# Kernel tuning notes

Measured on AMD Instinct MI355X. Metric: run time of the kernel, lower is better.

The kernel has to match this reference:

```python
import jax, jax.numpy as jnp
import numpy as np

N_NODES = 100000
N_EDGES = 1600000
IN_F, HID, N_COLORS = 128, 128, 10


def setup_inputs() -> dict:
    key = jax.random.key(0)
    k1, k2, k3, k4 = jax.random.split(key, 4)
    x = jax.random.normal(k1, (N_NODES, IN_F), dtype=jnp.float32)
    edge_index = jax.random.randint(k2, (2, N_EDGES), 0, N_NODES, dtype=jnp.int64)
    # Glorot-ish init for weights
    W1 = jax.random.normal(k3, (IN_F, HID), dtype=jnp.float32) / np.sqrt(IN_F)
    b1 = jnp.zeros((HID,), dtype=jnp.float32)
    W2 = jax.random.normal(k4, (HID, N_COLORS), dtype=jnp.float32) / np.sqrt(HID)
    b2 = jnp.zeros((N_COLORS,), dtype=jnp.float32)
    return {"x": x, "edge_index": edge_index, "W1": W1, "b1": b1, "W2": W2, "b2": b2}


def _gcn_norm(edge_index, num_nodes):
    # Add self-loops, compute symmetric normalization D^-1/2 (A+I) D^-1/2
    loops = jnp.arange(num_nodes, dtype=edge_index.dtype)
    src = jnp.concatenate([edge_index[0], loops])
    dst = jnp.concatenate([edge_index[1], loops])
    deg = jax.ops.segment_sum(jnp.ones_like(dst, dtype=jnp.float32), dst,
                              num_segments=num_nodes)
    deg_isqrt = jax.lax.rsqrt(deg)  # deg >= 1 due to self-loops
    norm = deg_isqrt[src] * deg_isqrt[dst]  # [E + N]
    return src, dst, norm


def _gcn_conv(h, src, dst, norm, num_nodes, W, b):
    # Linear transform first (PyG GCNConv), then gather-scale-scatter aggregate
    h = h @ W                                   # [N, out]
    msg = h[src] * norm[:, None]                # [E + N, out] gather
    out = jax.ops.segment_sum(msg, dst, num_segments=num_nodes)  # scatter-add
    return out + b


def reference(x, edge_index, W1, b1, W2, b2):
    n = x.shape[0]
    src, dst, norm = _gcn_norm(edge_index, n)
    h = _gcn_conv(x, src, dst, norm, n, W1, b1)
    h = jax.nn.relu(h)
    # dropout is identity in eval mode
    h = _gcn_conv(h, src, dst, norm, n, W2, b2)
    return jax.nn.softmax(h, axis=1)
```

## Files before the change

kernel.cpp:

```cpp
#include <hip/hip_runtime.h>
#include <hip/hip_fp16.h>

#define IN_F 128
#define HID  128
#define NC   10
#define H2P  16
#define NPB  128
#define NBMAX 784
#define BCAP 2560
#define CAPP 2944
#define EPB  4096

typedef _Float16 f16x8 __attribute__((ext_vector_type(8)));
typedef float f32x4 __attribute__((ext_vector_type(4)));
typedef int int4a __attribute__((ext_vector_type(4), aligned(4)));

__device__ inline __half2 shfl_xor_h2(__half2 v, int mask) {
    int i = __shfl_xor(*reinterpret_cast<int*>(&v), mask, 64);
    return *reinterpret_cast<__half2*>(&i);
}

__global__ __launch_bounds__(1024) void k_bin(const int* __restrict__ src,
                                              const int* __restrict__ dst,
                                              int* __restrict__ bcnt,
                                              unsigned int* __restrict__ binned,
                                              const float* __restrict__ W1,
                                              __half* __restrict__ WT,
                                              const float* __restrict__ W2,
                                              float* __restrict__ W2T,
                                              int E, int nbin) {
    __shared__ int hist[NBMAX];
    __shared__ int base[NBMAX];
    __shared__ int lcur[NBMAX];
    const int tid = threadIdx.x;

    if (blockIdx.x == 0) {
        for (int i = tid; i < IN_F * HID; i += 1024) {
            int k = i >> 7, n = i & 127;
            WT[n * IN_F + k] = __float2half(W1[k * HID + n]);
        }
        for (int i = tid; i < NC * IN_F; i += 1024)
            W2T[i] = W2[(i & 127) * NC + (i >> 7)];
    }

    for (int b = tid; b < nbin; b += 1024) { hist[b] = 0; lcur[b] = 0; }
    __syncthreads();

    const int e0 = blockIdx.x * EPB + tid;
    int d[4];
    #pragma unroll
    for (int u = 0; u < 4; u++) {
        int e = e0 + u * 1024;
        d[u] = (e < E) ? dst[e] : -1;
        if (d[u] >= 0) atomicAdd(&hist[d[u] >> 7], 1);
    }
    __syncthreads();
    for (int b = tid; b < nbin; b += 1024) {
        int h = hist[b];
        base[b] = h ? atomicAdd(&bcnt[b], h) : 0;
    }
    __syncthreads();
    #pragma unroll
    for (int u = 0; u < 4; u++) {
        int e = e0 + u * 1024;
        if (e < E) {
            int dd = d[u];
            int b = dd >> 7;
            int s = src[e];
            int o = base[b] + atomicAdd(&lcur[b], 1);
            if (o < BCAP)
                binned[(size_t)b * BCAP + o] = ((unsigned)(dd & 127) << 17) | (unsigned)s;
        }
    }
}

__global__ __launch_bounds__(256) void k_pg(const int* __restrict__ bcnt,
                                            const unsigned int* __restrict__ binned,
                                            int2* __restrict__ rowinfo,
                                            float* __restrict__ dis,
                                            int* __restrict__ csr,
                                            const float* __restrict__ X,
                                            const __half* __restrict__ WT,
                                            __half* __restrict__ hsh,
                                            __half* __restrict__ h2h,
                                            int N) {
    __shared__ int h[NPB];
    __shared__ int lb[NPB];
    __shared__ int cur[NPB];
    __shared__ float sdis[NPB];
    __shared__ _Float16 sX[32 * IN_F];
    __shared__ _Float16 sW[128 * IN_F];
    const int b = blockIdx.x;
    const int tid = threadIdx.x;

    if (tid < NPB) h[tid] = 0;
    __syncthreads();

    const int m = min(bcnt[b], BCAP);
    const unsigned int* p = binned + (size_t)b * BCAP;
    for (int i = tid; i < m; i += 256) atomicAdd(&h[p[i] >> 17], 1);
    __syncthreads();

    int myh = 0, cnt4 = 0;
    if (tid < NPB) { myh = h[tid]; cnt4 = (myh + 3) & ~3; lb[tid] = cnt4; }
    __syncthreads();
    #pragma unroll
    for (int off = 1; off < NPB; off <<= 1) {
        int t = (tid < NPB && tid >= off) ? lb[tid - off] : 0;
        __syncthreads();
        if (tid < NPB) lb[tid] += t;
        __syncthreads();
    }
    int ex = 0;
    if (tid < NPB) {
        ex = lb[tid] - cnt4;
        int node = b * NPB + tid;
        if (node < N) {
            rowinfo[node] = make_int2(b * CAPP + ex, cnt4);
            float dd = rsqrtf(1.0f + (float)myh);
            dis[node] = dd;
            sdis[tid] = dd;
        }
        lb[tid] = ex;
        cur[tid] = 0;
    }
    __syncthreads();
    for (int i = tid; i < m; i += 256) {
        unsigned v = p[i];
        int dl = v >> 17;
        int r = atomicAdd(&cur[dl], 1);
        csr[b * CAPP + lb[dl] + r] = (int)(v & 0x1FFFF);
    }
    if (tid < NPB) {
        for (int k = myh; k < cnt4; k++) csr[b * CAPP + ex + k] = N;
    }
    if (b == 0) {
        f16x8 z = {0, 0, 0, 0, 0, 0, 0, 0};
        if (tid < 16) *(f16x8*)(hsh + (size_t)N * HID + tid * 8) = z;
        if (tid < 2)  *(f16x8*)(h2h + (size_t)N * H2P + tid * 8) = z;
    }

    {
        int n = tid >> 1, part = tid & 1;
        const f16x8* srcp = (const f16x8*)(WT + n * IN_F + part * 64);
        f16x8* dstp = (f16x8*)(sW + n * IN_F + part * 64);
        #pragma unroll
        for (int c = 0; c < 8; c++) dstp[c] = srcp[c];
    }
    const int wave = tid >> 6;
    const int lane = tid & 63;
    const int quad = lane >> 4;
    const int l16 = lane & 15;
    const int nbase = wave * 32;

    for (int tdx = 0; tdx < 4; tdx++) {
        int row0 = b * NPB + tdx * 32;
        if (row0 >= N) break;
        __syncthreads();
        {
            int r = tid >> 3;
            int k0 = (tid & 7) * 16;
            const float* sp = X + (size_t)(row0 + r) * IN_F + k0;
            float4 f0 = *(const float4*)(sp);
            float4 f1 = *(const float4*)(sp + 4);
            float4 f2 = *(const float4*)(sp + 8);
            float4 f3 = *(const float4*)(sp + 12);
            f16x8 h0, h1;
            h0[0] = (_Float16)f0.x; h0[1] = (_Float16)f0.y;
            h0[2] = (_Float16)f0.z; h0[3] = (_Float16)f0.w;
            h0[4] = (_Float16)f1.x; h0[5] = (_Float16)f1.y;
            h0[6] = (_Float16)f1.z; h0[7] = (_Float16)f1.w;
            h1[0] = (_Float16)f2.x; h1[1] = (_Float16)f2.y;
            h1[2] = (_Float16)f2.z; h1[3] = (_Float16)f2.w;
            h1[4] = (_Float16)f3.x; h1[5] = (_Float16)f3.y;
            h1[6] = (_Float16)f3.z; h1[7] = (_Float16)f3.w;
            *(f16x8*)(sX + r * IN_F + k0) = h0;
            *(f16x8*)(sX + r * IN_F + k0 + 8) = h1;
        }
        __syncthreads();

        f32x4 acc00 = {0,0,0,0}, acc01 = {0,0,0,0}, acc10 = {0,0,0,0}, acc11 = {0,0,0,0};
        #pragma unroll
        for (int kc = 0; kc < 4; kc++) {
            const int koff = kc * 32 + quad * 8;
            f16x8 a0 = *(const f16x8*)(sX + l16 * IN_F + koff);
            f16x8 a1 = *(const f16x8*)(sX + (16 + l16) * IN_F + koff);
            f16x8 b0 = *(const f16x8*)(sW + (nbase + l16) * IN_F + koff);
            f16x8 b1 = *(const f16x8*)(sW + (nbase + 16 + l16) * IN_F + koff);
            acc00 = __builtin_amdgcn_mfma_f32_16x16x32_f16(a0, b0, acc00, 0, 0, 0);
            acc01 = __builtin_amdgcn_mfma_f32_16x16x32_f16(a0, b1, acc01, 0, 0, 0);
            acc10 = __builtin_amdgcn_mfma_f32_16x16x32_f16(a1, b0, acc10, 0, 0, 0);
            acc11 = __builtin_amdgcn_mfma_f32_16x16x32_f16(a1, b1, acc11, 0, 0, 0);
        }
        #pragma unroll
        for (int r = 0; r < 4; r++) {
            {
                int lr = tdx * 32 + quad * 4 + r;
                float d = sdis[lr];
                __half* o = hsh + (size_t)(b * NPB + lr) * HID + nbase + l16;
                o[0]  = __float2half(acc00[r] * d);
                o[16] = __float2half(acc01[r] * d);
            }
            {
                int lr = tdx * 32 + 16 + quad * 4 + r;
                float d = sdis[lr];
                __half* o = hsh + (size_t)(b * NPB + lr) * HID + nbase + l16;
                o[0]  = __float2half(acc10[r] * d);
                o[16] = __float2half(acc11[r] * d);
            }
        }
    }
}

__global__ __launch_bounds__(256) void k_agg1(const __half* __restrict__ hsh,
                                              const int2* __restrict__ rowinfo,
                                              const int* __restrict__ csr,
                                              const float* __restrict__ dis,
                                              const float* __restrict__ b1,
                                              const float* __restrict__ W2T,
                                              __half* __restrict__ h2h,
                                              int N) {
    __shared__ float sWT[NC][IN_F];
    for (int i = threadIdx.x; i < NC * IN_F; i += 256)
        ((float*)sWT)[i] = W2T[i];
    __syncthreads();

    const int node = blockIdx.x * 4 + (threadIdx.x >> 6);
    if (node >= N) return;
    const int lane = threadIdx.x & 63;
    const int g   = lane >> 4;
    const int l16 = lane & 15;
    const int f0  = l16 * 8;
    const __half2 hz = __half2half2(__float2half(0.0f));

    const int2 ri = rowinfo[node];
    const int beg = ri.x, end = ri.x + ri.y;

    __half2 acc2[4] = {hz, hz, hz, hz};
    if (g == 0) {
        float4 r = *(const float4*)(hsh + (size_t)node * HID + f0);
        const __half2* hh = (const __half2*)&r;
        acc2[0] = hh[0]; acc2[1] = hh[1]; acc2[2] = hh[2]; acc2[3] = hh[3];
    }

    for (int j0 = beg + 4 * g; j0 < end; j0 += 16) {
        int4a cv = *(const int4a*)(csr + j0);
        float4 r0 = *(const float4*)(hsh + (size_t)cv[0] * HID + f0);
        float4 r1 = *(const float4*)(hsh + (size_t)cv[1] * HID + f0);
        float4 r2 = *(const float4*)(hsh + (size_t)cv[2] * HID + f0);
        float4 r3 = *(const float4*)(hsh + (size_t)cv[3] * HID + f0);
        const __half2* h0 = (const __half2*)&r0;
        const __half2* h1 = (const __half2*)&r1;
        const __half2* h2 = (const __half2*)&r2;
        const __half2* h3 = (const __half2*)&r3;
        #pragma unroll
        for (int i = 0; i < 4; i++) {
            acc2[i] = __hadd2(acc2[i], h0[i]);
            acc2[i] = __hadd2(acc2[i], h1[i]);
            acc2[i] = __hadd2(acc2[i], h2[i]);
            acc2[i] = __hadd2(acc2[i], h3[i]);
        }
    }

    #pragma unroll
    for (int i = 0; i < 4; i++) {
        acc2[i] = __hadd2(acc2[i], shfl_xor_h2(acc2[i], 16));
        acc2[i] = __hadd2(acc2[i], shfl_xor_h2(acc2[i], 32));
    }
    float acc[8];
    #pragma unroll
    for (int i = 0; i < 4; i++) {
        float2 t = __half22float2(acc2[i]);
        acc[2 * i] = t.x; acc[2 * i + 1] = t.y;
    }

    const float d = dis[node];
    float4 ba = *(const float4*)(b1 + f0);
    float4 bb = *(const float4*)(b1 + f0 + 4);
    float h[8];
    h[0] = fmaxf(fmaf(d, acc[0], ba.x), 0.0f);
    h[1] = fmaxf(fmaf(d, acc[1], ba.y), 0.0f);
    h[2] = fmaxf(fmaf(d, acc[2], ba.z), 0.0f);
    h[3] = fmaxf(fmaf(d, acc[3], ba.w), 0.0f);
    h[4] = fmaxf(fmaf(d, acc[4], bb.x), 0.0f);
    h[5] = fmaxf(fmaf(d, acc[5], bb.y), 0.0f);
    h[6] = fmaxf(fmaf(d, acc[6], bb.z), 0.0f);
    h[7] = fmaxf(fmaf(d, acc[7], bb.w), 0.0f);

    const int cb = (g == 0) ? 0 : (g == 1) ? 3 : (g == 2) ? 6 : 8;
    const int nc = (g < 2) ? 3 : 2;
    float p[3];
    #pragma unroll
    for (int ci = 0; ci < 3; ci++) {
        if (ci < nc) {
            int c = cb + ci;
            float4 wa = *(const float4*)&sWT[c][f0];
            float4 wb = *(const float4*)&sWT[c][f0 + 4];
            float t = fmaf(h[0], wa.x, fmaf(h[1], wa.y, fmaf(h[2], wa.z, h[3] * wa.w)));
            t = fmaf(h[4], wb.x, fmaf(h[5], wb.y, fmaf(h[6], wb.z, fmaf(h[7], wb.w, t))));
            #pragma unroll
            for (int off = 1; off < 16; off <<= 1) t += __shfl_xor(t, off, 64);
            p[ci] = t;
        }
    }
    if (l16 == 0) {
        __half* o = h2h + (size_t)node * H2P + cb;
        for (int ci = 0; ci < nc; ci++) o[ci] = __float2half(d * p[ci]);
    }
}

__global__ __launch_bounds__(256) void k_agg2(const __half* __restrict__ h2h,
                                              const int2* __restrict__ rowinfo,
                                              const int* __restrict__ csr,
                                              const float* __restrict__ dis,
                                              const float* __restrict__ b2,
                                              float* __restrict__ out,
                                              int N) {
    int t = blockIdx.x * 256 + threadIdx.x;
    int node = t >> 3;
    if (node >= N) return;
    int o = t & 7;
    int q = o & 1;
    int eg = o >> 1;
    const int base = q * 8;
    const __half2 hz = __half2half2(__float2half(0.0f));

    __half2 a2[4] = {hz, hz, hz, hz};
    if (eg == 0) {
        float4 r = *(const float4*)(h2h + (size_t)node * H2P + base);
        const __half2* hh = (const __half2*)&r;
        a2[0] = hh[0]; a2[1] = hh[1]; a2[2] = hh[2]; a2[3] = hh[3];
    }
    const int2 ri = rowinfo[node];
    const int end = ri.x + ri.y;
    for (int j0 = ri.x + 4 * eg; j0 < end; j0 += 16) {
        int4a cv = *(const int4a*)(csr + j0);
        float4 r0 = *(const float4*)(h2h + (size_t)cv[0] * H2P + base);
        float4 r1 = *(const float4*)(h2h + (size_t)cv[1] * H2P + base);
        float4 r2 = *(const float4*)(h2h + (size_t)cv[2] * H2P + base);
        float4 r3 = *(const float4*)(h2h + (size_t)cv[3] * H2P + base);
        const __half2* h0 = (const __half2*)&r0;
        const __half2* h1 = (const __half2*)&r1;
        const __half2* h2 = (const __half2*)&r2;
        const __half2* h3 = (const __half2*)&r3;
        #pragma unroll
        for (int i = 0; i < 4; i++) {
            a2[i] = __hadd2(a2[i], h0[i]);
            a2[i] = __hadd2(a2[i], h1[i]);
            a2[i] = __hadd2(a2[i], h2[i]);
            a2[i] = __hadd2(a2[i], h3[i]);
        }
    }

    #pragma unroll
    for (int i = 0; i < 4; i++) {
        a2[i] = __hadd2(a2[i], shfl_xor_h2(a2[i], 2));
        a2[i] = __hadd2(a2[i], shfl_xor_h2(a2[i], 4));
    }

    float a[8];
    #pragma unroll
    for (int i = 0; i < 4; i++) {
        float2 tt = __half22float2(a2[i]);
        a[2 * i] = tt.x; a[2 * i + 1] = tt.y;
    }

    const float d = dis[node];
    float vv[8];
    #pragma unroll
    for (int i = 0; i < 8; i++) {
        int f = base + i;
        vv[i] = (f < NC) ? fmaf(d, a[i], b2[f]) : -1e30f;
    }
    float m = vv[0];
    #pragma unroll
    for (int i = 1; i < 8; i++) m = fmaxf(m, vv[i]);
    m = fmaxf(m, __shfl_xor(m, 1, 64));
    float e[8];
    float s = 0.0f;
    #pragma unroll
    for (int i = 0; i < 8; i++) { e[i] = (base + i < NC) ? expf(vv[i] - m) : 0.0f; s += e[i]; }
    s += __shfl_xor(s, 1, 64);
    float inv = 1.0f / s;

    float* op = out + (size_t)node * NC;
    if (o == 0) {
        *(float2*)(op + 0) = make_float2(e[0] * inv, e[1] * inv);
        *(float2*)(op + 2) = make_float2(e[2] * inv, e[3] * inv);
        *(float2*)(op + 4) = make_float2(e[4] * inv, e[5] * inv);
        *(float2*)(op + 6) = make_float2(e[6] * inv, e[7] * inv);
    } else if (o == 1) {
        *(float2*)(op + 8) = make_float2(e[0] * inv, e[1] * inv);
    }
}

extern "C" void kernel_launch(void* const* d_in, const int* in_sizes, int n_in,
                              void* d_out, int out_size, void* d_ws, size_t ws_size,
                              hipStream_t stream) {
    const float* x  = (const float*)d_in[0];
    const int*   ei = (const int*)d_in[1];
    const float* W1 = (const float*)d_in[2];
    const float* b1 = (const float*)d_in[3];
    const float* W2 = (const float*)d_in[4];
    const float* b2 = (const float*)d_in[5];
    float* out = (float*)d_out;

    const int N = in_sizes[0] / IN_F;
    const int E = in_sizes[1] / 2;
    const int* esrc = ei;
    const int* edst = ei + E;
    const int nbin = (N + NPB - 1) / NPB;

    char* ws = (char*)d_ws;
    int2*   rowinfo = (int2*)(ws);
    float*  dis     = (float*)(ws + 0x100000);
    int*    bcnt    = (int*)(ws + 0x180000);
    __half* WT      = (__half*)(ws + 0x190000);
    float*  W2T     = (float*)(ws + 0x1A0000);
    unsigned int* binned = (unsigned int*)(ws + 0x200000);
    int*    csr     = (int*)(ws + 0xA00000);
    __half* hsh     = (__half*)(ws + 0x1400000);
    __half* h2h     = (__half*)(ws + 0x2D00000);

    hipMemsetAsync(bcnt, 0, (size_t)nbin * sizeof(int), stream);

    k_bin <<<(E + EPB - 1) / EPB, 1024, 0, stream>>>(esrc, edst, bcnt, binned, W1, WT, W2, W2T, E, nbin);
    k_pg  <<<nbin, 256, 0, stream>>>(bcnt, binned, rowinfo, dis, csr, x, WT, hsh, h2h, N);
    k_agg1<<<(N + 3) / 4, 256, 0, stream>>>(hsh, rowinfo, csr, dis, b1, W2T, h2h, N);
    k_agg2<<<(int)(((size_t)N * 8 + 255) / 256), 256, 0, stream>>>(h2h, rowinfo, csr, dis, b2, out, N);
}
```

Measured before the change: 245.8 us.

## Split degree counting into prep kernel and co-schedule GEMM with edge binning

Adds a prep kernel that computes per-node degrees with global atomics and transposes the weights. A fused 'work' kernel then runs the dense X@W1 GEMM blocks alongside the edge-binning blocks, so the compute-bound and memory-bound phases overlap. A separate placement kernel builds the CSR from the precomputed degrees. The change also pads the shared-memory tiles to avoid bank conflicts, prefetches the next CSR index vector in agg1, and reads W2T directly from global memory instead of staging it in shared memory. The cost is an extra kernel launch and a full pass of global atomics over dst for the degrees.

Result: slower. 276.3 us (+12.4%).

```diff
diff --git a/kernel.cpp b/kernel.cpp
--- a/kernel.cpp
+++ b/kernel.cpp
@@ -10,6 +10,7 @@
 #define BCAP 2560
 #define CAPP 2944
 #define EPB  4096
+#define LDW  136
 
 typedef _Float16 f16x8 __attribute__((ext_vector_type(8)));
 typedef float f32x4 __attribute__((ext_vector_type(4)));
@@ -20,89 +21,185 @@
     return *reinterpret_cast<__half2*>(&i);
 }
 
-__global__ __launch_bounds__(1024) void k_bin(const int* __restrict__ src,
-                                              const int* __restrict__ dst,
-                                              int* __restrict__ bcnt,
-                                              unsigned int* __restrict__ binned,
-                                              const float* __restrict__ W1,
-                                              __half* __restrict__ WT,
-                                              const float* __restrict__ W2,
-                                              float* __restrict__ W2T,
-                                              int E, int nbin) {
-    __shared__ int hist[NBMAX];
-    __shared__ int base[NBMAX];
-    __shared__ int lcur[NBMAX];
+__global__ __launch_bounds__(1024) void k_prep(const int* __restrict__ dst,
+                                               int* __restrict__ deg,
+                                               const float* __restrict__ W1,
+                                               __half* __restrict__ WT,
+                                               const float* __restrict__ W2,
+                                               float* __restrict__ W2T,
+                                               __half* __restrict__ hsh,
+                                               __half* __restrict__ h2h,
+                                               int E, int N) {
+    const int gt = blockIdx.x * 1024 + threadIdx.x;
+    const int stride = gridDim.x * 1024;
+    for (int i = gt; i < IN_F * HID; i += stride) {
+        int k = i >> 7, n = i & 127;
+        WT[n * IN_F + k] = __float2half(W1[i]);
+    }
+    if (blockIdx.x == 0) {
+        for (int i = threadIdx.x; i < NC * IN_F; i += 1024)
+            W2T[i] = W2[(i & 127) * NC + (i >> 7)];
+        if (threadIdx.x < HID) hsh[(size_t)N * HID + threadIdx.x] = __float2half(0.0f);
+        if (threadIdx.x < H2P) h2h[(size_t)N * H2P + threadIdx.x] = __float2half(0.0f);
+    }
+    for (int i = gt; i < E; i += stride) atomicAdd(&deg[dst[i]], 1);
+}
+
+__global__ __launch_bounds__(1024, 4) void k_work(const int* __restrict__ src,
+                                                  const int* __restrict__ dst,
+                                                  int* __restrict__ bcnt,
+                                                  unsigned int* __restrict__ binned,
+                                                  const float* __restrict__ X,
+                                                  const __half* __restrict__ WT,
+                                                  const int* __restrict__ deg,
+                                                  float* __restrict__ dis,
+                                                  __half* __restrict__ hsh,
+                                                  int E, int nbin, int N, int NBG) {
+    __shared__ __align__(16) char smem[2 * 128 * LDW * 2 + 512];
     const int tid = threadIdx.x;
 
-    if (blockIdx.x == 0) {
-        for (int i = tid; i < IN_F * HID; i += 1024) {
-            int k = i >> 7, n = i & 127;
-            WT[n * IN_F + k] = __float2half(W1[k * HID + n]);
-        }
-        for (int i = tid; i < NC * IN_F; i += 1024)
-            W2T[i] = W2[(i & 127) * NC + (i >> 7)];
-    }
-
-    for (int b = tid; b < nbin; b += 1024) { hist[b] = 0; lcur[b] = 0; }
+    if (blockIdx.x >= NBG) {
+        int* hist = (int*)smem;
+        int* base = hist + NBMAX;
+        int* lcur = base + NBMAX;
+        for (int b = tid; b < nbin; b += 1024) { hist[b] = 0; lcur[b] = 0; }
+        __syncthreads();
+
+        const int e0 = (blockIdx.x - NBG) * EPB + tid;
+        int d[4];
+        #pragma unroll
+        for (int u = 0; u < 4; u++) {
+            int e = e0 + u * 1024;
+            d[u] = (e < E) ? dst[e] : -1;
+            if (d[u] >= 0) atomicAdd(&hist[d[u] >> 7], 1);
+        }
+        __syncthreads();
+        for (int b = tid; b < nbin; b += 1024) {
+            int h = hist[b];
+            base[b] = h ? atomicAdd(&bcnt[b], h) : 0;
+        }
+        __syncthreads();
+        #pragma unroll
+        for (int u = 0; u < 4; u++) {
+            int e = e0 + u * 1024;
+            if (e < E) {
+                int dd = d[u];
+                int b = dd >> 7;
+                int s = src[e];
+                int o = base[b] + atomicAdd(&lcur[b], 1);
+                if (o < BCAP)
+                    binned[(size_t)b * BCAP + o] = ((unsigned)(dd & 127) << 17) | (unsigned)s;
+            }
+        }
+        return;
+    }
+
+    _Float16* sX = (_Float16*)smem;
+    _Float16* sW = sX + 128 * LDW;
+    float* sdis  = (float*)(smem + 2 * 128 * LDW * 2);
+    const int row0 = blockIdx.x * 128;
+
+    {
+        int n = tid >> 3, c = tid & 7;
+        const f16x8* sp = (const f16x8*)(WT + n * IN_F);
+        *(f16x8*)(sW + n * LDW + c * 8)       = sp[c];
+        *(f16x8*)(sW + n * LDW + (c + 8) * 8) = sp[c + 8];
+    }
+    {
+        int r = tid >> 3;
+        int k0 = (tid & 7) * 16;
+        int row = row0 + r; if (row >= N) row = N - 1;
+        const float* sp = X + (size_t)row * IN_F + k0;
+        float4 f0 = *(const float4*)(sp);
+        float4 f1 = *(const float4*)(sp + 4);
+        float4 f2 = *(const float4*)(sp + 8);
+        float4 f3 = *(const float4*)(sp + 12);
+        f16x8 h0, h1;
+        h0[0] = (_Float16)f0.x; h0[1] = (_Float16)f0.y;
+        h0[2] = (_Float16)f0.z; h0[3] = (_Float16)f0.w;
+        h0[4] = (_Float16)f1.x; h0[5] = (_Float16)f1.y;
+        h0[6] = (_Float16)f1.z; h0[7] = (_Float16)f1.w;
+        h1[0] = (_Float16)f2.x; h1[1] = (_Float16)f2.y;
+        h1[2] = (_Float16)f2.z; h1[3] = (_Float16)f2.w;
+        h1[4] = (_Float16)f3.x; h1[5] = (_Float16)f3.y;
+        h1[6] = (_Float16)f3.z; h1[7] = (_Float16)f3.w;
+        *(f16x8*)(sX + r * LDW + k0) = h0;
+        *(f16x8*)(sX + r * LDW + k0 + 8) = h1;
+    }
+    if (tid < 128) {
+        int row = row0 + tid;
+        if (row < N) {
+            float dd = rsqrtf(1.0f + (float)deg[row]);
+            dis[row] = dd;
+            sdis[tid] = dd;
+        } else sdis[tid] = 0.0f;
+    }
     __syncthreads();
 
-    const int e0 = blockIdx.x * EPB + tid;
-    int d[4];
-    #pragma unroll
-    for (int u = 0; u < 4; u++) {
-        int e = e0 + u * 1024;
-        d[u] = (e < E) ? dst[e] : -1;
-        if (d[u] >= 0) atomicAdd(&hist[d[u] >> 7], 1);
-    }
-    __syncthreads();
-    for (int b = tid; b < nbin; b += 1024) {
-        int h = hist[b];
-        base[b] = h ? atomicAdd(&bcnt[b], h) : 0;
-    }
-    __syncthreads();
-    #pragma unroll
-    for (int u = 0; u < 4; u++) {
-        int e = e0 + u * 1024;
-        if (e < E) {
-            int dd = d[u];
-            int b = dd >> 7;
-            int s = src[e];
-            int o = base[b] + atomicAdd(&lcur[b], 1);
-            if (o < BCAP)
-                binned[(size_t)b * BCAP + o] = ((unsigned)(dd & 127) << 17) | (unsigned)s;
-        }
-    }
-}
-
-__global__ __launch_bounds__(256) void k_pg(const int* __restrict__ bcnt,
-                                            const unsigned int* __restrict__ binned,
-                                            int2* __restrict__ rowinfo,
-                                            float* __restrict__ dis,
-                                            int* __restrict__ csr,
-                                            const float* __restrict__ X,
-                                            const __half* __restrict__ WT,
-                                            __half* __restrict__ hsh,
-                                            __half* __restrict__ h2h,
-                                            int N) {
-    __shared__ int h[NPB];
+    const int wave = tid >> 6;
+    const int sub  = wave >> 2;
+    const int nbase = (wave & 3) * 32;
+    const int lane = tid & 63;
+    const int quad = lane >> 4;
+    const int l16 = lane & 15;
+    const int rbase = sub * 32;
+
+    f32x4 acc00 = {0,0,0,0}, acc01 = {0,0,0,0}, acc10 = {0,0,0,0}, acc11 = {0,0,0,0};
+    #pragma unroll
+    for (int kc = 0; kc < 4; kc++) {
+        const int koff = kc * 32 + quad * 8;
+        f16x8 a0 = *(const f16x8*)(sX + (rbase + l16) * LDW + koff);
+        f16x8 a1 = *(const f16x8*)(sX + (rbase + 16 + l16) * LDW + koff);
+        f16x8 b0 = *(const f16x8*)(sW + (nbase + l16) * LDW + koff);
+        f16x8 b1 = *(const f16x8*)(sW + (nbase + 16 + l16) * LDW + koff);
+        acc00 = __builtin_amdgcn_mfma_f32_16x16x32_f16(a0, b0, acc00, 0, 0, 0);
+        acc01 = __builtin_amdgcn_mfma_f32_16x16x32_f16(a0, b1, acc01, 0, 0, 0);
+        acc10 = __builtin_amdgcn_mfma_f32_16x16x32_f16(a1, b0, acc10, 0, 0, 0);
+        acc11 = __builtin_amdgcn_mfma_f32_16x16x32_f16(a1, b1, acc11, 0, 0, 0);
+    }
+    #pragma unroll
+    for (int r = 0; r < 4; r++) {
+        {
+            int lr = rbase + quad * 4 + r;
+            int row = row0 + lr;
+            if (row < N) {
+                float d = sdis[lr];
+                __half* o = hsh + (size_t)row * HID + nbase + l16;
+                o[0]  = __float2half(acc00[r] * d);
+                o[16] = __float2half(acc01[r] * d);
+            }
+        }
+        {
+            int lr = rbase + 16 + quad * 4 + r;
+            int row = row0 + lr;
+            if (row < N) {
+                float d = sdis[lr];
+                __half* o = hsh + (size_t)row * HID + nbase + l16;
+                o[0]  = __float2half(acc10[r] * d);
+                o[16] = __float2half(acc11[r] * d);
+            }
+        }
+    }
+}
+
+__global__ __launch_bounds__(256) void k_place(const int* __restrict__ bcnt,
+                                               const unsigned int* __restrict__ binned,
+                                               const int* __restrict__ deg,
+                                               int2* __restrict__ rowinfo,
+                                               int* __restrict__ csr,
+                                               int N) {
     __shared__ int lb[NPB];
     __shared__ int cur[NPB];
-    __shared__ float sdis[NPB];
-    __shared__ _Float16 sX[32 * IN_F];
-    __shared__ _Float16 sW[128 * IN_F];
     const int b = blockIdx.x;
     const int tid = threadIdx.x;
 
-    if (tid < NPB) h[tid] = 0;
-    __syncthreads();
-
-    const int m = min(bcnt[b], BCAP);
-    const unsigned int* p = binned + (size_t)b * BCAP;
-    for (int i = tid; i < m; i += 256) atomicAdd(&h[p[i] >> 17], 1);
-    __syncthreads();
-
     int myh = 0, cnt4 = 0;
-    if (tid < NPB) { myh = h[tid]; cnt4 = (myh + 3) & ~3; lb[tid] = cnt4; }
+    if (tid < NPB) {
+        int node = b * NPB + tid;
+        myh = (node < N) ? deg[node] : 0;
+        cnt4 = (myh + 3) & ~3;
+        lb[tid] = cnt4;
+    }
     __syncthreads();
     #pragma unroll
     for (int off = 1; off < NPB; off <<= 1) {
@@ -115,16 +212,13 @@
     if (tid < NPB) {
         ex = lb[tid] - cnt4;
         int node = b * NPB + tid;
-        if (node < N) {
-            rowinfo[node] = make_int2(b * CAPP + ex, cnt4);
-            float dd = rsqrtf(1.0f + (float)myh);
-            dis[node] = dd;
-            sdis[tid] = dd;
-        }
+        if (node < N) rowinfo[node] = make_int2(b * CAPP + ex, cnt4);
         lb[tid] = ex;
         cur[tid] = 0;
     }
     __syncthreads();
+    const int m = min(bcnt[b], BCAP);
+    const unsigned int* p = binned + (size_t)b * BCAP;
     for (int i = tid; i < m; i += 256) {
         unsigned v = p[i];
         int dl = v >> 17;
@@ -133,82 +227,6 @@
     }
     if (tid < NPB) {
         for (int k = myh; k < cnt4; k++) csr[b * CAPP + ex + k] = N;
-    }
-    if (b == 0) {
-        f16x8 z = {0, 0, 0, 0, 0, 0, 0, 0};
-        if (tid < 16) *(f16x8*)(hsh + (size_t)N * HID + tid * 8) = z;
-        if (tid < 2)  *(f16x8*)(h2h + (size_t)N * H2P + tid * 8) = z;
-    }
-
-    {
-        int n = tid >> 1, part = tid & 1;
-        const f16x8* srcp = (const f16x8*)(WT + n * IN_F + part * 64);
-        f16x8* dstp = (f16x8*)(sW + n * IN_F + part * 64);
-        #pragma unroll
-        for (int c = 0; c < 8; c++) dstp[c] = srcp[c];
-    }
-    const int wave = tid >> 6;
-    const int lane = tid & 63;
-    const int quad = lane >> 4;
-    const int l16 = lane & 15;
-    const int nbase = wave * 32;
-
-    for (int tdx = 0; tdx < 4; tdx++) {
-        int row0 = b * NPB + tdx * 32;
-        if (row0 >= N) break;
-        __syncthreads();
-        {
-            int r = tid >> 3;
-            int k0 = (tid & 7) * 16;
-            const float* sp = X + (size_t)(row0 + r) * IN_F + k0;
-            float4 f0 = *(const float4*)(sp);
-            float4 f1 = *(const float4*)(sp + 4);
-            float4 f2 = *(const float4*)(sp + 8);
-            float4 f3 = *(const float4*)(sp + 12);
-            f16x8 h0, h1;
-            h0[0] = (_Float16)f0.x; h0[1] = (_Float16)f0.y;
-            h0[2] = (_Float16)f0.z; h0[3] = (_Float16)f0.w;
-            h0[4] = (_Float16)f1.x; h0[5] = (_Float16)f1.y;
-            h0[6] = (_Float16)f1.z; h0[7] = (_Float16)f1.w;
-            h1[0] = (_Float16)f2.x; h1[1] = (_Float16)f2.y;
-            h1[2] = (_Float16)f2.z; h1[3] = (_Float16)f2.w;
-            h1[4] = (_Float16)f3.x; h1[5] = (_Float16)f3.y;
-            h1[6] = (_Float16)f3.z; h1[7] = (_Float16)f3.w;
-            *(f16x8*)(sX + r * IN_F + k0) = h0;
-            *(f16x8*)(sX + r * IN_F + k0 + 8) = h1;
-        }
-        __syncthreads();
-
-        f32x4 acc00 = {0,0,0,0}, acc01 = {0,0,0,0}, acc10 = {0,0,0,0}, acc11 = {0,0,0,0};
-        #pragma unroll
-        for (int kc = 0; kc < 4; kc++) {
-            const int koff = kc * 32 + quad * 8;
-            f16x8 a0 = *(const f16x8*)(sX + l16 * IN_F + koff);
-            f16x8 a1 = *(const f16x8*)(sX + (16 + l16) * IN_F + koff);
-            f16x8 b0 = *(const f16x8*)(sW + (nbase + l16) * IN_F + koff);
-            f16x8 b1 = *(const f16x8*)(sW + (nbase + 16 + l16) * IN_F + koff);
-            acc00 = __builtin_amdgcn_mfma_f32_16x16x32_f16(a0, b0, acc00, 0, 0, 0);
-            acc01 = __builtin_amdgcn_mfma_f32_16x16x32_f16(a0, b1, acc01, 0, 0, 0);
-            acc10 = __builtin_amdgcn_mfma_f32_16x16x32_f16(a1, b0, acc10, 0, 0, 0);
-            acc11 = __builtin_amdgcn_mfma_f32_16x16x32_f16(a1, b1, acc11, 0, 0, 0);
-        }
-        #pragma unroll
-        for (int r = 0; r < 4; r++) {
-            {
-                int lr = tdx * 32 + quad * 4 + r;
-                float d = sdis[lr];
-                __half* o = hsh + (size_t)(b * NPB + lr) * HID + nbase + l16;
-                o[0]  = __float2half(acc00[r] * d);
-                o[16] = __float2half(acc01[r] * d);
-            }
-            {
-                int lr = tdx * 32 + 16 + quad * 4 + r;
-                float d = sdis[lr];
-                __half* o = hsh + (size_t)(b * NPB + lr) * HID + nbase + l16;
-                o[0]  = __float2half(acc10[r] * d);
-                o[16] = __float2half(acc11[r] * d);
-            }
-        }
     }
 }
 
@@ -220,11 +238,6 @@
                                               const float* __restrict__ W2T,
                                               __half* __restrict__ h2h,
                                               int N) {
-    __shared__ float sWT[NC][IN_F];
-    for (int i = threadIdx.x; i < NC * IN_F; i += 256)
-        ((float*)sWT)[i] = W2T[i];
-    __syncthreads();
-
     const int node = blockIdx.x * 4 + (threadIdx.x >> 6);
     if (node >= N) return;
     const int lane = threadIdx.x & 63;
@@ -235,6 +248,7 @@
 
     const int2 ri = rowinfo[node];
     const int beg = ri.x, end = ri.x + ri.y;
+    const float d = dis[node];
 
     __half2 acc2[4] = {hz, hz, hz, hz};
     if (g == 0) {
@@ -243,22 +257,31 @@
         acc2[0] = hh[0]; acc2[1] = hh[1]; acc2[2] = hh[2]; acc2[3] = hh[3];
     }
 
-    for (int j0 = beg + 4 * g; j0 < end; j0 += 16) {
+    int j0 = beg + 4 * g;
+    if (j0 < end) {
         int4a cv = *(const int4a*)(csr + j0);
-        float4 r0 = *(const float4*)(hsh + (size_t)cv[0] * HID + f0);
-        float4 r1 = *(const float4*)(hsh + (size_t)cv[1] * HID + f0);
-        float4 r2 = *(const float4*)(hsh + (size_t)cv[2] * HID + f0);
-        float4 r3 = *(const float4*)(hsh + (size_t)cv[3] * HID + f0);
-        const __half2* h0 = (const __half2*)&r0;
-        const __half2* h1 = (const __half2*)&r1;
-        const __half2* h2 = (const __half2*)&r2;
-        const __half2* h3 = (const __half2*)&r3;
-        #pragma unroll
-        for (int i = 0; i < 4; i++) {
-            acc2[i] = __hadd2(acc2[i], h0[i]);
-            acc2[i] = __hadd2(acc2[i], h1[i]);
-            acc2[i] = __hadd2(acc2[i], h2[i]);
-            acc2[i] = __hadd2(acc2[i], h3[i]);
+        while (true) {
+            const int jn = j0 + 16;
+            const bool more = (jn < end);
+            int4a cvn = cv;
+            if (more) cvn = *(const int4a*)(csr + jn);
+            float4 r0 = *(const float4*)(hsh + (size_t)cv[0] * HID + f0);
+            float4 r1 = *(const float4*)(hsh + (size_t)cv[1] * HID + f0);
+            float4 r2 = *(const float4*)(hsh + (size_t)cv[2] * HID + f0);
+            float4 r3 = *(const float4*)(hsh + (size_t)cv[3] * HID + f0);
+            const __half2* h0 = (const __half2*)&r0;
+            const __half2* h1 = (const __half2*)&r1;
+            const __half2* h2 = (const __half2*)&r2;
+            const __half2* h3 = (const __half2*)&r3;
+            #pragma unroll
+            for (int i = 0; i < 4; i++) {
+                acc2[i] = __hadd2(acc2[i], h0[i]);
+                acc2[i] = __hadd2(acc2[i], h1[i]);
+                acc2[i] = __hadd2(acc2[i], h2[i]);
+                acc2[i] = __hadd2(acc2[i], h3[i]);
+            }
+            if (!more) break;
+            cv = cvn; j0 = jn;
         }
     }
 
@@ -274,7 +297,6 @@
         acc[2 * i] = t.x; acc[2 * i + 1] = t.y;
     }
 
-    const float d = dis[node];
     float4 ba = *(const float4*)(b1 + f0);
     float4 bb = *(const float4*)(b1 + f0 + 4);
     float h[8];
@@ -294,8 +316,8 @@
     for (int ci = 0; ci < 3; ci++) {
         if (ci < nc) {
             int c = cb + ci;
-            float4 wa = *(const float4*)&sWT[c][f0];
-            float4 wb = *(const float4*)&sWT[c][f0 + 4];
+            float4 wa = *(const float4*)(W2T + c * IN_F + f0);
+            float4 wb = *(const float4*)(W2T + c * IN_F + f0 + 4);
             float t = fmaf(h[0], wa.x, fmaf(h[1], wa.y, fmaf(h[2], wa.z, h[3] * wa.w)));
             t = fmaf(h[4], wb.x, fmaf(h[5], wb.y, fmaf(h[6], wb.z, fmaf(h[7], wb.w, t))));
             #pragma unroll
@@ -410,22 +432,27 @@
     const int* esrc = ei;
     const int* edst = ei + E;
     const int nbin = (N + NPB - 1) / NPB;
+    const int NBG  = (N + 127) / 128;
+    const int NBB  = (E + EPB - 1) / EPB;
 
     char* ws = (char*)d_ws;
     int2*   rowinfo = (int2*)(ws);
     float*  dis     = (float*)(ws + 0x100000);
-    int*    bcnt    = (int*)(ws + 0x180000);
-    __half* WT      = (__half*)(ws + 0x190000);
-    float*  W2T     = (float*)(ws + 0x1A0000);
+    int*    deg     = (int*)(ws + 0x180000);
+    int*    bcnt    = (int*)(ws + 0x1E2000);
+    __half* WT      = (__half*)(ws + 0x1F0000);
+    float*  W2T     = (float*)(ws + 0x1F8000);
     unsigned int* binned = (unsigned int*)(ws + 0x200000);
     int*    csr     = (int*)(ws + 0xA00000);
     __half* hsh     = (__half*)(ws + 0x1400000);
     __half* h2h     = (__half*)(ws + 0x2D00000);
 
-    hipMemsetAsync(bcnt, 0, (size_t)nbin * sizeof(int), stream);
-
-    k_bin <<<(E + EPB - 1) / EPB, 1024, 0, stream>>>(esrc, edst, bcnt, binned, W1, WT, W2, W2T, E, nbin);
-    k_pg  <<<nbin, 256, 0, stream>>>(bcnt, binned, rowinfo, dis, csr, x, WT, hsh, h2h, N);
-    k_agg1<<<(N + 3) / 4, 256, 0, stream>>>(hsh, rowinfo, csr, dis, b1, W2T, h2h, N);
-    k_agg2<<<(int)(((size_t)N * 8 + 255) / 256), 256, 0, stream>>>(h2h, rowinfo, csr, dis, b2, out, N);
-}
+    hipMemsetAsync(deg, 0, 0x62000 + (size_t)nbin * sizeof(int), stream);
+
+    k_prep <<<400, 1024, 0, stream>>>(edst, deg, W1, WT, W2, W2T, hsh, h2h, E, N);
+    k_work <<<NBG + NBB, 1024, 0, stream>>>(esrc, edst, bcnt, binned, x, WT, deg, dis, hsh,
+                                            E, nbin, N, NBG);
+    k_place<<<nbin, 256, 0, stream>>>(bcnt, binned, deg, rowinfo, csr, N);
+    k_agg1 <<<(N + 3) / 4, 256, 0, stream>>>(hsh, rowinfo, csr, dis, b1, W2T, h2h, N);
+    k_agg2 <<<(int)(((size_t)N * 8 + 255) / 256), 256, 0, stream>>>(h2h, rowinfo, csr, dis, b2, out, N);
+}
```
